# Optimization experiments

Hardware: AMD Instinct MI355X
Metric: run time of the kernel (lower is better)

## Reference

```python
import jax, jax.numpy as jnp
import numpy as np

N, E = 100000, 1600000
H, F, G = 128, 128, 51   # hidden_channels, num_filters, num_gaussians
CUTOFF = 10.0
LOG2 = 0.6931471805599453

def ssp(x):
    # ShiftedSoftplus: softplus(x) - log(2)
    return jax.nn.softplus(x) - jnp.asarray(LOG2, x.dtype)

def setup_inputs() -> dict:
    key = jax.random.key(0)
    ks = jax.random.split(key, 16)
    s = 0.05
    return {
        "z": jax.random.normal(ks[0], (N, H), dtype=jnp.float32),
        "pos": jax.random.uniform(ks[1], (N, 3), dtype=jnp.float32),
        "edge_index": jax.random.randint(ks[2], (2, E), 0, N, dtype=jnp.int64),
        # CFConv linears
        "lin1_w": jax.random.normal(ks[3], (F, H), dtype=jnp.float32) * s,   # no bias
        "lin2_w": jax.random.normal(ks[4], (H, F), dtype=jnp.float32) * s,
        "lin2_b": jnp.zeros((H,), dtype=jnp.float32),
        # edge-filter MLP: Linear(G,F) -> ssp -> Linear(F,F)
        "mlp0_w": jax.random.normal(ks[5], (F, G), dtype=jnp.float32) * s,
        "mlp0_b": jnp.zeros((F,), dtype=jnp.float32),
        "mlp2_w": jax.random.normal(ks[6], (F, F), dtype=jnp.float32) * s,
        "mlp2_b": jnp.zeros((F,), dtype=jnp.float32),
        # InteractionBlock output linear
        "blk_w": jax.random.normal(ks[7], (H, H), dtype=jnp.float32) * s,
        "blk_b": jnp.zeros((H,), dtype=jnp.float32),
        # SchNetLayer head: lin1 -> ssp -> lin2
        "out1_w": jax.random.normal(ks[8], (H, H), dtype=jnp.float32) * s,
        "out1_b": jnp.zeros((H,), dtype=jnp.float32),
        "out2_w": jax.random.normal(ks[9], (H, H), dtype=jnp.float32) * s,
        "out2_b": jnp.zeros((H,), dtype=jnp.float32),
    }

def reference(z, pos, edge_index, lin1_w, lin2_w, lin2_b, mlp0_w, mlp0_b,
              mlp2_w, mlp2_b, blk_w, blk_b, out1_w, out1_b, out2_w, out2_b):
    row, col = edge_index[0], edge_index[1]
    # edge distances
    d = pos[row] - pos[col]                          # [E,3]
    ew = jnp.sqrt(jnp.sum(d * d, axis=-1) + 1e-12)   # [E]
    # GaussianSmearing(0, cutoff, G)
    offset = jnp.linspace(0.0, CUTOFF, G).astype(ew.dtype)
    coeff = -0.5 / (CUTOFF / (G - 1)) ** 2
    ea = jnp.exp(coeff * (ew[:, None] - offset[None, :]) ** 2)  # [E,G]
    # cosine cutoff envelope
    C = 0.5 * (jnp.cos(ew * (jnp.pi / CUTOFF)) + 1.0)           # [E]
    # edge-conditioned filter W = mlp(edge_attr) * C
    W = ssp(ea @ mlp0_w.T + mlp0_b) @ mlp2_w.T + mlp2_b         # [E,F]
    W = W * C[:, None]
    # CFConv: lin1 -> gather(x_j) * W -> scatter-add -> lin2
    x1 = z @ lin1_w.T                                            # [N,F]
    msg = x1[row] * W                                            # [E,F]
    agg = jax.ops.segment_sum(msg, col, num_segments=z.shape[0]) # [N,F]
    conv = agg @ lin2_w.T + lin2_b                               # [N,H]
    # InteractionBlock: act -> lin, residual add
    h = z + (ssp(conv) @ blk_w.T + blk_b)
    # head: lin1 -> ssp -> lin2
    h = ssp(h @ out1_w.T + out1_b) @ out2_w.T + out2_b
    return h
```

## Files before the change

### kernel.cpp

```cpp
#include <hip/hip_runtime.h>
#include <math.h>


#define HDIM 128
#define GDIM 51
#define TAB_T 2048
#define TAB_PTS (TAB_T + 1)
#define RMAX 1.7330f
#define INV_STEP ((float)TAB_T / RMAX)
#define WMAT 2048
#define SCB 2048

typedef short short8 __attribute__((ext_vector_type(8)));
typedef float floatx4 __attribute__((ext_vector_type(4)));

__device__ __forceinline__ float ssp_f(float x) {
  float t = __expf(-fabsf(x));
  return fmaxf(x, 0.0f) + __logf(1.0f + t) - 0.6931471805599453f;
}
__device__ __forceinline__ float bl(unsigned int u) { return __uint_as_float(u << 16); }
__device__ __forceinline__ float bh(unsigned int u) { return __uint_as_float(u & 0xFFFF0000u); }
__device__ __forceinline__ unsigned short f2bf(float f) {
  unsigned int u = __float_as_uint(f);
  unsigned int r = u + 0x7FFFu + ((u >> 16) & 1u);
  return (unsigned short)(r >> 16);
}
__device__ __forceinline__ unsigned int pack_bf16(float a, float b) {
  unsigned int r;
  asm("v_cvt_pk_bf16_f32 %0, %1, %2" : "=v"(r) : "v"(a), "v"(b));
  return r;
}

__global__ void prep_kernel(const float* __restrict__ lin1, const float* __restrict__ lin2,
                            const float* __restrict__ blkw, const float* __restrict__ o1w,
                            const float* __restrict__ o2w, const float* __restrict__ m0w,
                            const float* __restrict__ m2w,
                            unsigned short* __restrict__ wbf,
                            float* __restrict__ m0t, float* __restrict__ m2t) {
  int gid = blockIdx.x * blockDim.x + threadIdx.x;
  int stride = gridDim.x * blockDim.x;
  for (int idx = gid; idx < 5 * 16384; idx += stride) {
    int mat = idx >> 14;
    int o   = idx & 16383;
    int idx4 = o >> 3;
    int jj   = o & 7;
    int ct   = idx4 >> 8;
    int kk   = (idx4 >> 6) & 3;
    int lane = idx4 & 63;
    int c = ct * 16 + (lane & 15);
    int g = kk * 4 + (lane >> 4);
    const float* w = (mat == 0) ? lin1 : (mat == 1) ? lin2 : (mat == 2) ? blkw
                   : (mat == 3) ? o1w : o2w;
    wbf[idx] = f2bf(w[c * HDIM + g * 8 + jj]);
  }
  for (int idx = gid; idx < GDIM * HDIM; idx += stride) {
    int g = idx >> 7, f = idx & 127;
    m0t[idx] = m0w[f * GDIM + g];
  }
  for (int idx = gid; idx < HDIM * HDIM; idx += stride) {
    int j = idx >> 7, f = idx & 127;
    m2t[idx] = m2w[f * HDIM + j];
  }
}

__global__ __launch_bounds__(128) void table_kernel(
    const float* __restrict__ m0t, const float* __restrict__ m0b,
    const float* __restrict__ m2t, const float* __restrict__ m2b,
    unsigned int* __restrict__ tab2) {
  __shared__ float ea[GDIM];
  __shared__ float h1[HDIM];
  int f = threadIdx.x;
  float b0 = m0b[f];
  float b2 = m2b[f];
  for (int t = blockIdx.x; t < TAB_PTS; t += gridDim.x) {
    float ew = (float)t * (RMAX / (float)TAB_T);
    if (f < GDIM) {
      float dd = ew - (float)f * 0.2f;
      ea[f] = expf(-12.5f * dd * dd);
    }
    __syncthreads();
    float s = b0;
    #pragma unroll 3
    for (int g = 0; g < GDIM; ++g) s = fmaf(ea[g], m0t[g * HDIM + f], s);
    h1[f] = ssp_f(s);
    __syncthreads();
    float s2 = b2;
    #pragma unroll 4
    for (int j = 0; j < HDIM; ++j) s2 = fmaf(h1[j], m2t[j * HDIM + f], s2);
    float C = 0.5f * (cosf(ew * 0.31415926535897931f) + 1.0f);
    float val = s2 * C;
    float pr = __shfl_xor(val, 1);
    if ((f & 1) == 0) {
      unsigned int w = pack_bf16(val, pr);
      int c = f >> 1;
      if (t < TAB_T) tab2[(size_t)t * 128 + c * 2] = w;
      if (t > 0)     tab2[(size_t)(t - 1) * 128 + c * 2 + 1] = w;
    }
    __syncthreads();
  }
}

__device__ __forceinline__ short8 frag_ld(const unsigned int* __restrict__ slab,
                                          int row, int g) {
  const uint4 v = *(const uint4*)(slab + row * 64 + (((g << 2) ^ ((row & 7) << 2))));
  return __builtin_bit_cast(short8, v);
}

__device__ __forceinline__ void stage_act64(unsigned int* __restrict__ slab,
                                            const float* __restrict__ src,
                                            int n0, int N, int t) {
  #pragma unroll
  for (int i = 0; i < 8; ++i) {
    int id = t + i * 256;
    int r  = id >> 5;
    int k4 = id & 31;
    int gn = n0 + r;
    float4 v = make_float4(0.f, 0.f, 0.f, 0.f);
    if (gn < N) v = *(const float4*)(src + (size_t)gn * HDIM + k4 * 4);
    int w = (k4 * 2) ^ ((r & 7) * 4);
    *(uint2*)(slab + r * 64 + w) = make_uint2(pack_bf16(v.x, v.y), pack_bf16(v.z, v.w));
  }
}

__device__ __forceinline__ void stage_mm8(const unsigned int* __restrict__ Aslab,
                                          const uint4* __restrict__ wm,
                                          floatx4 acc[8], int wave, int lane) {
  int m = lane & 15, q = lane >> 4;
  int r0 = wave * 16 + m;
  #pragma unroll
  for (int ct = 0; ct < 8; ++ct) acc[ct] = (floatx4){0.f, 0.f, 0.f, 0.f};
  #pragma unroll
  for (int kk = 0; kk < 4; ++kk) {
    short8 a = frag_ld(Aslab, r0, kk * 4 + q);
    #pragma unroll
    for (int ct = 0; ct < 8; ++ct) {
      short8 b = __builtin_bit_cast(short8, wm[(ct * 4 + kk) * 64 + lane]);
      acc[ct] = __builtin_amdgcn_mfma_f32_16x16x32_bf16(a, b, acc[ct], 0, 0, 0);
    }
  }
}

__device__ __forceinline__ void mm_cs1(const unsigned int* __restrict__ Aslab,
                                       const uint4* __restrict__ wm,
                                       floatx4 acc[4], int ct, int lane) {
  int m = lane & 15, q = lane >> 4;
  #pragma unroll
  for (int mr = 0; mr < 4; ++mr) acc[mr] = (floatx4){0.f, 0.f, 0.f, 0.f};
  #pragma unroll
  for (int kk = 0; kk < 4; ++kk) {
    short8 b = __builtin_bit_cast(short8, wm[(ct * 4 + kk) * 64 + lane]);
    #pragma unroll
    for (int mr = 0; mr < 4; ++mr) {
      short8 a = frag_ld(Aslab, mr * 16 + m, kk * 4 + q);
      acc[mr] = __builtin_amdgcn_mfma_f32_16x16x32_bf16(a, b, acc[mr], 0, 0, 0);
    }
  }
}

__device__ __forceinline__ void wb_cs1(unsigned int* __restrict__ slab,
                                       const floatx4 acc[4], float bias,
                                       int ct, int lane, bool do_ssp) {
  int m = lane & 15, q = lane >> 4;
  bool act = ((m ^ ct) & 1) == 0;
  int k2 = ct * 8 + (m >> 1);
  #pragma unroll
  for (int mr = 0; mr < 4; ++mr) {
    #pragma unroll
    for (int r = 0; r < 4; ++r) {
      float v = acc[mr][r] + bias;
      if (do_ssp) v = ssp_f(v);
      float pr = __shfl_xor(v, 1);
      if (act) {
        int R = mr * 16 + q * 4 + r;
        slab[R * 64 + (k2 ^ ((R & 7) * 4))] = (m & 1) ? pack_bf16(pr, v)
                                                      : pack_bf16(v, pr);
      }
    }
  }
}

__global__ __launch_bounds__(256) void x1_kernel(const float* __restrict__ z,
    const uint4* __restrict__ wbf4, unsigned int* __restrict__ x1b, int N) {
  __shared__ unsigned int Aslab[64 * 64];
  int t = threadIdx.x, wave = t >> 6, lane = t & 63;
  int m = lane & 15, q = lane >> 4;
  int n0 = blockIdx.x * 64;
  stage_act64(Aslab, z, n0, N, t);
  __syncthreads();
  floatx4 acc[8];
  stage_mm8(Aslab, wbf4, acc, wave, lane);
  #pragma unroll
  for (int ct = 0; ct < 8; ++ct) {
    #pragma unroll
    for (int r = 0; r < 4; ++r) {
      float v = acc[ct][r];
      float pr = __shfl_xor(v, 1);
      int gr = n0 + wave * 16 + q * 4 + r;
      if (((m ^ ct) & 1) == 0 && gr < N)
        x1b[(size_t)gr * 64 + ct * 8 + (m >> 1)] = (m & 1) ? pack_bf16(pr, v)
                                                           : pack_bf16(v, pr);
    }
  }
}

__global__ __launch_bounds__(256) void edge_kernel(const int* __restrict__ ei,
    const float* __restrict__ pos, int* __restrict__ count,
    unsigned int* __restrict__ erec, int* __restrict__ erank, int E) {
  int gid = blockIdx.x * blockDim.x + threadIdx.x;
  int stride = gridDim.x * blockDim.x;
  for (int e = gid; e < E; e += stride) {
    int row = ei[e];
    int col = ei[E + e];
    float dx = pos[row * 3]     - pos[col * 3];
    float dy = pos[row * 3 + 1] - pos[col * 3 + 1];
    float dz = pos[row * 3 + 2] - pos[col * 3 + 2];
    float ew = sqrtf(dx * dx + dy * dy + dz * dz + 1e-12f);
    float u = ew * INV_STEP;
    int t0 = min((int)u, TAB_T - 1);
    float fr = u - (float)t0;
    int f4 = min((int)(fr * 16.0f), 15);
    erec[e] = ((unsigned int)row << 15) | ((unsigned int)t0 << 4)
            | (unsigned int)f4;
    erank[e] = atomicAdd(&count[col], 1);
  }
}

__global__ __launch_bounds__(256) void scan1_kernel(const int* __restrict__ count,
                                                    int* __restrict__ bsum, int N) {
  int b = blockIdx.x, t = threadIdx.x;
  int base = b * SCB;
  int s = 0;
  for (int i = t; i < SCB; i += 256) {
    int gi = base + i;
    s += (gi < N) ? count[gi] : 0;
  }
  #pragma unroll
  for (int d = 32; d >= 1; d >>= 1) s += __shfl_down(s, d);
  __shared__ int ws[4];
  if ((t & 63) == 0) ws[t >> 6] = s;
  __syncthreads();
  if (t == 0) bsum[b] = ws[0] + ws[1] + ws[2] + ws[3];
}

__global__ __launch_bounds__(64) void scan2_kernel(const int* __restrict__ bsum,
    int* __restrict__ boff, int* __restrict__ startN, int NB) {
  int lane = threadIdx.x;
  int carry = 0;
  for (int base = 0; base < NB; base += 64) {
    int i = base + lane;
    int v = (i < NB) ? bsum[i] : 0;
    int x = v;
    #pragma unroll
    for (int d = 1; d < 64; d <<= 1) {
      int y = __shfl_up(x, d);
      if (lane >= d) x += y;
    }
    if (i < NB) boff[i] = carry + x - v;
    carry += __shfl(x, 63);
  }
  if (lane == 0) *startN = carry;
}

__global__ __launch_bounds__(256) void scan3_kernel(const int* __restrict__ count,
    const int* __restrict__ boff, int* __restrict__ start, int N) {
  int b = blockIdx.x, t = threadIdx.x;
  int lane = t & 63, w = t >> 6;
  int loc = b * SCB + t * 8;
  int v[8];
  int s = 0;
  #pragma unroll
  for (int j = 0; j < 8; ++j) {
    int gi = loc + j;
    v[j] = (gi < N) ? count[gi] : 0;
    s += v[j];
  }
  int x = s;
  #pragma unroll
  for (int d = 1; d < 64; d <<= 1) {
    int y = __shfl_up(x, d);
    if (lane >= d) x += y;
  }
  __shared__ int ws[4];
  if (lane == 63) ws[w] = x;
  __syncthreads();
  int wbase = 0;
  #pragma unroll
  for (int k = 0; k < 3; ++k) wbase += (k < w) ? ws[k] : 0;
  int excl = boff[b] + wbase + x - s;
  #pragma unroll
  for (int j = 0; j < 8; ++j) {
    int gi = loc + j;
    if (gi < N) start[gi] = excl;
    excl += v[j];
  }
}

__global__ __launch_bounds__(256) void perm_kernel(const int* __restrict__ ei,
    const unsigned int* __restrict__ erec, const int* __restrict__ erank,
    const int* __restrict__ start, unsigned int* __restrict__ srec, int E) {
  int gid = blockIdx.x * blockDim.x + threadIdx.x;
  int stride = gridDim.x * blockDim.x;
  for (int e = gid; e < E; e += stride) {
    int col = ei[E + e];
    srec[start[col] + erank[e]] = erec[e];
  }
}

__device__ __forceinline__ void edge_math(unsigned int xw, uint2 w01, float fr,
                                          float& ax, float& ay) {
  float wa = fmaf(fr, bl(w01.y) - bl(w01.x), bl(w01.x));
  float wb = fmaf(fr, bh(w01.y) - bh(w01.x), bh(w01.x));
  ax = fmaf(bl(xw), wa, ax);
  ay = fmaf(bh(xw), wb, ay);
}

__global__ __launch_bounds__(256) void agg_kernel(const unsigned int* __restrict__ srec,
    const int* __restrict__ start, const unsigned int* __restrict__ x1b,
    const uint2* __restrict__ tab2, unsigned int* __restrict__ aggb, int N) {
  int wid = __builtin_amdgcn_readfirstlane(
      (int)((blockIdx.x * 256 + threadIdx.x) >> 6));
  int lane = threadIdx.x & 63;
  if (wid >= N) return;
  int s = __builtin_amdgcn_readfirstlane(start[wid]);
  int e = __builtin_amdgcn_readfirstlane(start[wid + 1]);
  float ax = 0.f, ay = 0.f;
  int i = s;
  for (; i + 8 <= e; i += 8) {
    unsigned int xw[8];
    uint2 w01[8];
    float fr[8];
    #pragma unroll
    for (int j = 0; j < 8; ++j) {
      unsigned int rec = __builtin_amdgcn_readfirstlane(srec[i + j]);
      int row = (int)(rec >> 15);
      int t0  = (int)((rec >> 4) & 2047u);
      fr[j] = (float)(rec & 15u) * 0.0625f + 0.03125f;
      xw[j]  = (x1b  + ((unsigned)row << 6))[lane];
      w01[j] = (tab2 + ((unsigned)t0  << 6))[lane];
    }
    #pragma unroll
    for (int j = 0; j < 8; ++j) edge_math(xw[j], w01[j], fr[j], ax, ay);
  }
  for (; i < e; ++i) {
    unsigned int rec = __builtin_amdgcn_readfirstlane(srec[i]);
    int row = (int)(rec >> 15);
    int t0  = (int)((rec >> 4) & 2047u);
    float fr = (float)(rec & 15u) * 0.0625f + 0.03125f;
    unsigned int xw = (x1b + ((unsigned)row << 6))[lane];
    uint2 w01 = (tab2 + ((unsigned)t0 << 6))[lane];
    edge_math(xw, w01, fr, ax, ay);
  }
  aggb[(size_t)wid * 64 + lane] = pack_bf16(ax, ay);
}

__global__ __launch_bounds__(512) void epilogue_kernel(
    const unsigned int* __restrict__ aggb, const float* __restrict__ z,
    const uint4* __restrict__ wbf4,
    const float* __restrict__ b_lin2, const float* __restrict__ b_blk,
    const float* __restrict__ b_o1, const float* __restrict__ b_o2,
    float* __restrict__ out, int N) {
  __shared__ unsigned int Aslab[2][64 * 64];
  int t = threadIdx.x, wave = t >> 6, lane = t & 63;
  int m = lane & 15, q = lane >> 4;
  int n0 = blockIdx.x * 64;
  int ct = wave;
  bool act = ((m ^ ct) & 1) == 0;
  int k2 = ct * 8 + (m >> 1);
  int cb = ct * 16 + (m & ~1);
  floatx4 acc[4];

  float bs1 = b_lin2[ct * 16 + m];
  float bs2 = b_blk [ct * 16 + m];
  float bs3 = b_o1  [ct * 16 + m];
  float bs4 = b_o2  [ct * 16 + m];

  #pragma unroll
  for (int i = 0; i < 4; ++i) {
    int id = t + i * 512;
    int r  = id >> 5;
    int k22 = id & 31;
    int gn = n0 + r;
    uint2 v = make_uint2(0u, 0u);
    if (gn < N) v = *(const uint2*)(aggb + (size_t)gn * 64 + k22 * 2);
    *(uint2*)(Aslab[0] + r * 64 + ((k22 * 2) ^ ((r & 7) * 4))) = v;
  }
  __syncthreads();

  mm_cs1(Aslab[0], wbf4 + 1 * WMAT, acc, ct, lane);
  wb_cs1(Aslab[1], acc, bs1, ct, lane, true);
  __syncthreads();

  mm_cs1(Aslab[1], wbf4 + 2 * WMAT, acc, ct, lane);
  #pragma unroll
  for (int mr = 0; mr < 4; ++mr) {
    #pragma unroll
    for (int r = 0; r < 4; ++r) {
      int gr = n0 + mr * 16 + q * 4 + r;
      float2 zz = make_float2(0.f, 0.f);
      if (act && gr < N) zz = *(const float2*)(z + (size_t)gr * HDIM + cb);
      float mine  = (m & 1) ? zz.y : zz.x;
      float yours = (m & 1) ? zz.x : zz.y;
      float other = __shfl_xor(yours, 1);
      float zval = act ? mine : other;
      float v = acc[mr][r] + bs2 + zval;
      float pr = __shfl_xor(v, 1);
      if (act) {
        int R = mr * 16 + q * 4 + r;
        Aslab[0][R * 64 + (k2 ^ ((R & 7) * 4))] = (m & 1) ? pack_bf16(pr, v)
                                                          : pack_bf16(v, pr);
      }
    }
  }
  __syncthreads();

  mm_cs1(Aslab[0], wbf4 + 3 * WMAT, acc, ct, lane);
  wb_cs1(Aslab[1], acc, bs3, ct, lane, true);
  __syncthreads();

  mm_cs1(Aslab[1], wbf4 + 4 * WMAT, acc, ct, lane);
  #pragma unroll
  for (int mr = 0; mr < 4; ++mr) {
    #pragma unroll
    for (int r = 0; r < 4; ++r) {
      float v = acc[mr][r] + bs4;
      float pr = __shfl_xor(v, 1);
      int gr = n0 + mr * 16 + q * 4 + r;
      if (act && gr < N) {
        float lo = (m & 1) ? pr : v;
        float hi = (m & 1) ? v : pr;
        *(float2*)(out + (size_t)gr * HDIM + cb) = make_float2(lo, hi);
      }
    }
  }
}

extern "C" void kernel_launch(void* const* d_in, const int* in_sizes, int n_in,
                              void* d_out, int out_size, void* d_ws, size_t ws_size,
                              hipStream_t stream) {
  const float* z     = (const float*)d_in[0];
  const float* pos   = (const float*)d_in[1];
  const int*   ei    = (const int*)d_in[2];
  const float* lin1  = (const float*)d_in[3];
  const float* lin2  = (const float*)d_in[4];
  const float* blin2 = (const float*)d_in[5];
  const float* m0w   = (const float*)d_in[6];
  const float* m0b   = (const float*)d_in[7];
  const float* m2w   = (const float*)d_in[8];
  const float* m2b   = (const float*)d_in[9];
  const float* blkw  = (const float*)d_in[10];
  const float* blkb  = (const float*)d_in[11];
  const float* o1w   = (const float*)d_in[12];
  const float* o1b   = (const float*)d_in[13];
  const float* o2w   = (const float*)d_in[14];
  const float* o2b   = (const float*)d_in[15];
  float* out = (float*)d_out;
  const int N = in_sizes[0] / HDIM;
  const int E = in_sizes[2] / 2;
  const int NB = (N + SCB - 1) / SCB;

  char* wsb = (char*)d_ws;
  size_t off = 0;
  auto alloc = [&](size_t bytes) {
    void* p = wsb + off;
    off += (bytes + 15) & ~(size_t)15;
    return p;
  };
  unsigned int* x1b  = (unsigned int*)alloc((size_t)N * 64 * 4);
  unsigned int* aggb = (unsigned int*)alloc((size_t)N * 64 * 4);
  unsigned int* tab2 = (unsigned int*)alloc((size_t)TAB_T * 128 * 4);
  float* m0t  = (float*)alloc((size_t)GDIM * HDIM * 4);
  float* m2t  = (float*)alloc((size_t)HDIM * HDIM * 4);
  unsigned short* wbf = (unsigned short*)alloc(5 * 16384 * 2);
  int* count  = (int*)alloc(((size_t)N + 1) * 4);
  int* start  = (int*)alloc(((size_t)N + 1) * 4);
  int* bsum   = (int*)alloc(((size_t)NB + 1) * 4);
  int* boff   = (int*)alloc(((size_t)NB + 1) * 4);
  unsigned int* srec  = (unsigned int*)alloc((size_t)E * 4);
  unsigned int* erec  = (unsigned int*)alloc((size_t)E * 4);
  int*          erank = (int*)alloc((size_t)E * 4);

  const int ngrid = (N + 63) / 64;
  prep_kernel<<<256, 256, 0, stream>>>(lin1, lin2, blkw, o1w, o2w, m0w, m2w,
                                       wbf, m0t, m2t);
  hipMemsetAsync(count, 0, ((size_t)N + 1) * 4, stream);
  edge_kernel<<<2048, 256, 0, stream>>>(ei, pos, count, erec, erank, E);
  scan1_kernel<<<NB, 256, 0, stream>>>(count, bsum, N);
  scan2_kernel<<<1, 64, 0, stream>>>(bsum, boff, start + N, NB);
  scan3_kernel<<<NB, 256, 0, stream>>>(count, boff, start, N);
  perm_kernel<<<2048, 256, 0, stream>>>(ei, erec, erank, start, srec, E);
  table_kernel<<<512, 128, 0, stream>>>(m0t, m0b, m2t, m2b, tab2);
  x1_kernel<<<ngrid, 256, 0, stream>>>(z, (const uint4*)wbf, x1b, N);
  agg_kernel<<<(N + 3) / 4, 256, 0, stream>>>(srec, start, x1b,
                                              (const uint2*)tab2, aggb, N);
  epilogue_kernel<<<ngrid, 512, 0, stream>>>(aggb, z, (const uint4*)wbf, blin2,
                                             blkb, o1b, o2b, out, N);
}
```

Measured before the change: 425.4 us.

## Sub-bucket edges by source row range within each destination for gather locality

The counting sort now keys edges by destination node and by the high bits of the source row, splitting each destination into 16 buckets. Within each destination's edge list, sources therefore appear in roughly ascending blocks. Concurrent waves then gather x1 rows from similar regions, which is meant to improve cache hit rates in the aggregation. The cost is a count/start array 16x larger, giving a bigger memset and longer scans, plus more atomic keys.

```diff
diff --git a/kernel.cpp b/kernel.cpp
--- a/kernel.cpp
+++ b/kernel.cpp
@@ -10,6 +10,8 @@
 #define INV_STEP ((float)TAB_T / RMAX)
 #define WMAT 2048
 #define SCB 2048
+#define NBK 16
+#define BSH 13
 
 typedef short short8 __attribute__((ext_vector_type(8)));
 typedef float floatx4 __attribute__((ext_vector_type(4)));
@@ -221,18 +223,19 @@
     int f4 = min((int)(fr * 16.0f), 15);
     erec[e] = ((unsigned int)row << 15) | ((unsigned int)t0 << 4)
             | (unsigned int)f4;
-    erank[e] = atomicAdd(&count[col], 1);
+    int key = col * NBK + (row >> BSH);
+    erank[e] = atomicAdd(&count[key], 1);
   }
 }
 
 __global__ __launch_bounds__(256) void scan1_kernel(const int* __restrict__ count,
-                                                    int* __restrict__ bsum, int N) {
+                                                    int* __restrict__ bsum, int N2) {
   int b = blockIdx.x, t = threadIdx.x;
   int base = b * SCB;
   int s = 0;
   for (int i = t; i < SCB; i += 256) {
     int gi = base + i;
-    s += (gi < N) ? count[gi] : 0;
+    s += (gi < N2) ? count[gi] : 0;
   }
   #pragma unroll
   for (int d = 32; d >= 1; d >>= 1) s += __shfl_down(s, d);
@@ -262,7 +265,7 @@
 }
 
 __global__ __launch_bounds__(256) void scan3_kernel(const int* __restrict__ count,
-    const int* __restrict__ boff, int* __restrict__ start, int N) {
+    const int* __restrict__ boff, int* __restrict__ start, int N2) {
   int b = blockIdx.x, t = threadIdx.x;
   int lane = t & 63, w = t >> 6;
   int loc = b * SCB + t * 8;
@@ -271,7 +274,7 @@
   #pragma unroll
   for (int j = 0; j < 8; ++j) {
     int gi = loc + j;
-    v[j] = (gi < N) ? count[gi] : 0;
+    v[j] = (gi < N2) ? count[gi] : 0;
     s += v[j];
   }
   int x = s;
@@ -290,7 +293,7 @@
   #pragma unroll
   for (int j = 0; j < 8; ++j) {
     int gi = loc + j;
-    if (gi < N) start[gi] = excl;
+    if (gi < N2) start[gi] = excl;
     excl += v[j];
   }
 }
@@ -302,7 +305,9 @@
   int stride = gridDim.x * blockDim.x;
   for (int e = gid; e < E; e += stride) {
     int col = ei[E + e];
-    srec[start[col] + erank[e]] = erec[e];
+    unsigned int rec = erec[e];
+    int key = col * NBK + (int)((rec >> 15) >> BSH);
+    srec[start[key] + erank[e]] = rec;
   }
 }
 
@@ -321,8 +326,8 @@
       (int)((blockIdx.x * 256 + threadIdx.x) >> 6));
   int lane = threadIdx.x & 63;
   if (wid >= N) return;
-  int s = __builtin_amdgcn_readfirstlane(start[wid]);
-  int e = __builtin_amdgcn_readfirstlane(start[wid + 1]);
+  int s = __builtin_amdgcn_readfirstlane(start[wid * NBK]);
+  int e = __builtin_amdgcn_readfirstlane(start[wid * NBK + NBK]);
   float ax = 0.f, ay = 0.f;
   int i = s;
   for (; i + 8 <= e; i += 8) {
@@ -456,7 +461,8 @@
   float* out = (float*)d_out;
   const int N = in_sizes[0] / HDIM;
   const int E = in_sizes[2] / 2;
-  const int NB = (N + SCB - 1) / SCB;
+  const int N2 = N * NBK;
+  const int NB = (N2 + SCB - 1) / SCB;
 
   char* wsb = (char*)d_ws;
   size_t off = 0;
@@ -471,8 +477,8 @@
   float* m0t  = (float*)alloc((size_t)GDIM * HDIM * 4);
   float* m2t  = (float*)alloc((size_t)HDIM * HDIM * 4);
   unsigned short* wbf = (unsigned short*)alloc(5 * 16384 * 2);
-  int* count  = (int*)alloc(((size_t)N + 1) * 4);
-  int* start  = (int*)alloc(((size_t)N + 1) * 4);
+  int* count  = (int*)alloc(((size_t)N2 + 1) * 4);
+  int* start  = (int*)alloc(((size_t)N2 + 1) * 4);
   int* bsum   = (int*)alloc(((size_t)NB + 1) * 4);
   int* boff   = (int*)alloc(((size_t)NB + 1) * 4);
   unsigned int* srec  = (unsigned int*)alloc((size_t)E * 4);
@@ -482,11 +488,11 @@
   const int ngrid = (N + 63) / 64;
   prep_kernel<<<256, 256, 0, stream>>>(lin1, lin2, blkw, o1w, o2w, m0w, m2w,
                                        wbf, m0t, m2t);
-  hipMemsetAsync(count, 0, ((size_t)N + 1) * 4, stream);
+  hipMemsetAsync(count, 0, ((size_t)N2 + 1) * 4, stream);
   edge_kernel<<<2048, 256, 0, stream>>>(ei, pos, count, erec, erank, E);
-  scan1_kernel<<<NB, 256, 0, stream>>>(count, bsum, N);
-  scan2_kernel<<<1, 64, 0, stream>>>(bsum, boff, start + N, NB);
-  scan3_kernel<<<NB, 256, 0, stream>>>(count, boff, start, N);
+  scan1_kernel<<<NB, 256, 0, stream>>>(count, bsum, N2);
+  scan2_kernel<<<1, 64, 0, stream>>>(bsum, boff, start + N2, NB);
+  scan3_kernel<<<NB, 256, 0, stream>>>(count, boff, start, N2);
   perm_kernel<<<2048, 256, 0, stream>>>(ei, erec, erank, start, srec, E);
   table_kernel<<<512, 128, 0, stream>>>(m0t, m0b, m2t, m2b, tab2);
   x1_kernel<<<ngrid, 256, 0, stream>>>(z, (const uint4*)wbf, x1b, N);
```

Measured after the change: 453.1 us. 6.5% more time.
